# Kernel optimization log

Hardware: AMD Instinct MI355X
Metric: run time of the kernel (lower is better)

Reference implementation:

```python
import jax, jax.numpy as jnp
import numpy as np
import math

B, N, F_IN, F_OUT = 16, 2048, 256, 64


def setup_inputs() -> dict:
    key = jax.random.key(0)
    k1, k2, k3, k4 = jax.random.split(key, 4)
    x = jax.random.normal(k1, (B, N, F_IN), dtype=jnp.float32)
    adj = jax.random.randint(k2, (B, N, N), 0, 2, dtype=jnp.int32)
    stdv = 1.0 / math.sqrt(F_OUT)
    weight = jax.random.uniform(k3, (F_IN, F_OUT), dtype=jnp.float32, minval=-stdv, maxval=stdv)
    # weight2 stdv = 1/sqrt(1) = 1.0
    weight2 = jax.random.uniform(k4, (2 * F_OUT, 1), dtype=jnp.float32, minval=-1.0, maxval=1.0)
    return {"x": x, "adj": adj, "weight": weight, "weight2": weight2}


def reference(x, adj, weight, weight2):
    # h[b,n,o] = (x @ weight)  -- shared linear projection
    h = jnp.einsum("bni,io->bno", x, weight)
    Fo = weight.shape[1]
    # Split additive-attention vector: e_ij = relu(h_i . a_src + h_j . a_dst)
    # Mathematically identical to cat([h_i, h_j]) @ weight2 of the original.
    a_src = weight2[:Fo, 0]
    a_dst = weight2[Fo:, 0]
    s_src = jnp.einsum("bno,o->bn", h, a_src)  # [B, N]
    s_dst = jnp.einsum("bno,o->bn", h, a_dst)  # [B, N]
    e = jax.nn.relu(s_src[:, :, None] + s_dst[:, None, :])  # [B, N, N]
    NEG = jnp.float32(-9e15)
    scores = jnp.where(adj > 0, e, NEG)
    attention = jax.nn.softmax(scores, axis=2)  # softmax over neighbors j
    # dropout = 0.0 / eval mode -> identity
    out = jnp.einsum("bij,bjo->bio", attention, h)  # [B, N, F_OUT]
    return out
```

## Files before the change

kernel.cpp:

```cpp
#include <hip/hip_runtime.h>
#include <hip/hip_bf16.h>

#define BB 16
#define NN 2048
#define FIN 256
#define FO 64
#define PADW 264
#define CH 256

typedef __bf16 bf16x8 __attribute__((ext_vector_type(8)));
typedef __bf16 bf16x4 __attribute__((ext_vector_type(4)));
typedef float  f32x4  __attribute__((ext_vector_type(4)));
typedef int    i32x4  __attribute__((ext_vector_type(4)));

__global__ __launch_bounds__(256) void k1_gemm(
    const float* __restrict__ x, const float* __restrict__ weight,
    const float* __restrict__ w2,
    __bf16* __restrict__ hT, float* __restrict__ s_src, float* __restrict__ s_dst) {
    __shared__ __bf16 WtL[FO * PADW];
    __shared__ float vsL[FIN], vdL[FIN];
    int t = threadIdx.x;
    {
        const float4* wr = (const float4*)(weight + t * FO);
        float a = 0.f, d = 0.f;
#pragma unroll
        for (int c = 0; c < 16; ++c) {
            float4 v = wr[c];
            int o = c * 4;
            WtL[(o + 0) * PADW + t] = (__bf16)v.x;
            WtL[(o + 1) * PADW + t] = (__bf16)v.y;
            WtL[(o + 2) * PADW + t] = (__bf16)v.z;
            WtL[(o + 3) * PADW + t] = (__bf16)v.w;
            a += v.x * w2[o] + v.y * w2[o + 1] + v.z * w2[o + 2] + v.w * w2[o + 3];
            d += v.x * w2[FO + o] + v.y * w2[FO + o + 1] +
                 v.z * w2[FO + o + 2] + v.w * w2[FO + o + 3];
        }
        vsL[t] = a;
        vdL[t] = d;
    }
    __syncthreads();

    int lane = threadIdx.x & 63, w = threadIdx.x >> 6;
    int quad = lane >> 4, m = lane & 15;
    int Rbase = blockIdx.x * 64 + w * 16;
    int R = Rbase + m;
    const float* xr = x + (long)R * FIN;

    f32x4 acc[4] = {};
    float ps = 0.f, pd = 0.f;

#pragma unroll
    for (int k0 = 0; k0 < FIN; k0 += 32) {
        int kb = k0 + quad * 8;
        float4 x0 = *(const float4*)(xr + kb);
        float4 x1 = *(const float4*)(xr + kb + 4);
        float4 u0 = *(const float4*)(vsL + kb);
        float4 u1 = *(const float4*)(vsL + kb + 4);
        float4 t0 = *(const float4*)(vdL + kb);
        float4 t1 = *(const float4*)(vdL + kb + 4);
        ps += x0.x * u0.x + x0.y * u0.y + x0.z * u0.z + x0.w * u0.w +
              x1.x * u1.x + x1.y * u1.y + x1.z * u1.z + x1.w * u1.w;
        pd += x0.x * t0.x + x0.y * t0.y + x0.z * t0.z + x0.w * t0.w +
              x1.x * t1.x + x1.y * t1.y + x1.z * t1.z + x1.w * t1.w;
        bf16x8 bf = {(__bf16)x0.x, (__bf16)x0.y, (__bf16)x0.z, (__bf16)x0.w,
                     (__bf16)x1.x, (__bf16)x1.y, (__bf16)x1.z, (__bf16)x1.w};
#pragma unroll
        for (int ot = 0; ot < 4; ++ot) {
            bf16x8 af = *(const bf16x8*)(WtL + (ot * 16 + m) * PADW + kb);
            acc[ot] = __builtin_amdgcn_mfma_f32_16x16x32_bf16(af, bf, acc[ot], 0, 0, 0);
        }
    }
    ps += __shfl_xor(ps, 16);
    ps += __shfl_xor(ps, 32);
    pd += __shfl_xor(pd, 16);
    pd += __shfl_xor(pd, 32);
    if (quad == 0) {
        s_src[R] = ps;
        s_dst[R] = pd;
    }
    int b = R >> 11;
    int nb = Rbase & (NN - 1);
#pragma unroll
    for (int ot = 0; ot < 4; ++ot) {
#pragma unroll
        for (int r = 0; r < 4; ++r) {
            int o = ot * 16 + quad * 4 + r;
            hT[((long)b * FO + o) * NN + nb + m] = (__bf16)acc[ot][r];
        }
    }
}

__global__ __launch_bounds__(256) void k2_attn(
    const int* __restrict__ adj, const float* __restrict__ s_src,
    const float* __restrict__ s_dst, const __bf16* __restrict__ hT,
    float* __restrict__ out) {
    __shared__ __bf16 pbuf[4][16 * CH];
    int b = blockIdx.x >> 5;
    int i0 = (blockIdx.x & 31) << 6;
    int lane = threadIdx.x & 63, w = threadIdx.x >> 6;
    int quad = lane >> 4, m = lane & 15;
    int rowbase = i0 + w * 16;

    const float* sd = s_dst + b * NN;
    float mx = -3.0e38f;
    for (int j = lane; j < NN; j += 64) mx = fmaxf(mx, sd[j]);
#pragma unroll
    for (int off = 32; off >= 1; off >>= 1) mx = fmaxf(mx, __shfl_xor(mx, off));

    const float* ssp = s_src + b * NN + rowbase;
    const int* adjb = adj + ((long)b * NN + rowbase) * NN;
    const __bf16* hTb = hT + (long)b * FO * NN;
    __bf16* pb = pbuf[w];

    f32x4 acc[4] = {};
    f32x4 accL = {};
    const bf16x8 ones = {(__bf16)1.f, (__bf16)1.f, (__bf16)1.f, (__bf16)1.f,
                         (__bf16)1.f, (__bf16)1.f, (__bf16)1.f, (__bf16)1.f};
    int g0 = lane >> 3, u = (lane & 7) * 4;

    for (int jc = 0; jc < NN; jc += CH) {
        float4 sv = *(const float4*)(sd + jc + 4 * lane);
#pragma unroll
        for (int r = 0; r < 16; ++r) {
            float sr = ssp[r];
            float M = fmaxf(sr + mx, 0.f);
            i32x4 a0 = __builtin_nontemporal_load(
                (const i32x4*)(adjb + (long)r * NN + jc) + lane);
            float p0 = (a0.x > 0) ? __expf(fmaxf(sr + sv.x, 0.f) - M) : 0.f;
            float p1 = (a0.y > 0) ? __expf(fmaxf(sr + sv.y, 0.f) - M) : 0.f;
            float p2 = (a0.z > 0) ? __expf(fmaxf(sr + sv.z, 0.f) - M) : 0.f;
            float p3 = (a0.w > 0) ? __expf(fmaxf(sr + sv.w, 0.f) - M) : 0.f;
            bf16x4 kv = {(__bf16)p0, (__bf16)p1, (__bf16)p2, (__bf16)p3};
            *(bf16x4*)(pb + g0 * 512 + r * 32 + u) = kv;
        }
#pragma unroll
        for (int ks = 0; ks < CH / 32; ++ks) {
            bf16x8 af = *(const bf16x8*)(pb + ks * 512 + m * 32 + quad * 8);
            accL = __builtin_amdgcn_mfma_f32_16x16x32_bf16(af, ones, accL, 0, 0, 0);
            const __bf16* hb = hTb + jc + ks * 32 + quad * 8;
#pragma unroll
            for (int ot = 0; ot < 4; ++ot) {
                bf16x8 bf = *(const bf16x8*)(hb + (ot * 16 + m) * NN);
                acc[ot] = __builtin_amdgcn_mfma_f32_16x16x32_bf16(af, bf, acc[ot], 0, 0, 0);
            }
        }
    }

    float* outp = out + ((long)b * NN + rowbase) * FO;
#pragma unroll
    for (int r = 0; r < 4; ++r) {
        int orow = quad * 4 + r;
        float inv = 1.0f / accL[r];
#pragma unroll
        for (int ot = 0; ot < 4; ++ot) {
            outp[(long)orow * FO + ot * 16 + m] = acc[ot][r] * inv;
        }
    }
}

extern "C" void kernel_launch(void* const* d_in, const int* in_sizes, int n_in,
                              void* d_out, int out_size, void* d_ws, size_t ws_size,
                              hipStream_t stream) {
    const float* x      = (const float*)d_in[0];
    const int*   adj    = (const int*)d_in[1];
    const float* weight = (const float*)d_in[2];
    const float* w2     = (const float*)d_in[3];
    float* out = (float*)d_out;

    char* ws = (char*)d_ws;
    __bf16* hT   = (__bf16*)ws;
    float* s_src = (float*)(ws + 4194304);
    float* s_dst = (float*)(ws + 4194304 + 131072);

    k1_gemm<<<512, 256, 0, stream>>>(x, weight, w2, hT, s_src, s_dst);
    k2_attn<<<512, 256, 0, stream>>>(adj, s_src, s_dst, hT, out);
}
```

Before: 476.9 us.

## Pre-pack adjacency into a bitmask and compute attention probabilities directly in registers

A new streaming kernel converts the int32 adjacency matrix into a 1-bit-per-edge mask. The attention kernel then loads each row's mask once and distributes words via lane shuffles. It builds bf16 probability fragments in registers instead of staging them through LDS, and caches s_dst in shared memory. This decouples the bandwidth-heavy adjacency read from the exp/MFMA loop, at the cost of an extra kernel launch and a small mask write/read.

```diff
diff --git a/kernel.cpp b/kernel.cpp
--- a/kernel.cpp
+++ b/kernel.cpp
@@ -5,19 +5,17 @@
 #define NN 2048
 #define FIN 256
 #define FO 64
-#define PADW 264
-#define CH 256
 
 typedef __bf16 bf16x8 __attribute__((ext_vector_type(8)));
-typedef __bf16 bf16x4 __attribute__((ext_vector_type(4)));
 typedef float  f32x4  __attribute__((ext_vector_type(4)));
 typedef int    i32x4  __attribute__((ext_vector_type(4)));
+typedef unsigned int uint;
 
 __global__ __launch_bounds__(256) void k1_gemm(
     const float* __restrict__ x, const float* __restrict__ weight,
     const float* __restrict__ w2,
     __bf16* __restrict__ hT, float* __restrict__ s_src, float* __restrict__ s_dst) {
-    __shared__ __bf16 WtL[FO * PADW];
+    __shared__ __bf16 WtL[FO * 264];
     __shared__ float vsL[FIN], vdL[FIN];
     int t = threadIdx.x;
     {
@@ -27,10 +25,10 @@
         for (int c = 0; c < 16; ++c) {
             float4 v = wr[c];
             int o = c * 4;
-            WtL[(o + 0) * PADW + t] = (__bf16)v.x;
-            WtL[(o + 1) * PADW + t] = (__bf16)v.y;
-            WtL[(o + 2) * PADW + t] = (__bf16)v.z;
-            WtL[(o + 3) * PADW + t] = (__bf16)v.w;
+            WtL[(o + 0) * 264 + t] = (__bf16)v.x;
+            WtL[(o + 1) * 264 + t] = (__bf16)v.y;
+            WtL[(o + 2) * 264 + t] = (__bf16)v.z;
+            WtL[(o + 3) * 264 + t] = (__bf16)v.w;
             a += v.x * w2[o] + v.y * w2[o + 1] + v.z * w2[o + 2] + v.w * w2[o + 3];
             d += v.x * w2[FO + o] + v.y * w2[FO + o + 1] +
                  v.z * w2[FO + o + 2] + v.w * w2[FO + o + 3];
@@ -66,7 +64,7 @@
                      (__bf16)x1.x, (__bf16)x1.y, (__bf16)x1.z, (__bf16)x1.w};
 #pragma unroll
         for (int ot = 0; ot < 4; ++ot) {
-            bf16x8 af = *(const bf16x8*)(WtL + (ot * 16 + m) * PADW + kb);
+            bf16x8 af = *(const bf16x8*)(WtL + (ot * 16 + m) * 264 + kb);
             acc[ot] = __builtin_amdgcn_mfma_f32_16x16x32_bf16(af, bf, acc[ot], 0, 0, 0);
         }
     }
@@ -90,54 +88,80 @@
     }
 }
 
+__global__ __launch_bounds__(256) void k_pack(const int* __restrict__ adj,
+                                              unsigned char* __restrict__ mask) {
+    size_t t = (size_t)blockIdx.x * 256 + threadIdx.x;
+    const i32x4* ap = (const i32x4*)(adj + t * 8);
+    i32x4 a0 = __builtin_nontemporal_load(ap);
+    i32x4 a1 = __builtin_nontemporal_load(ap + 1);
+    unsigned b = (unsigned)(a0.x > 0) | ((unsigned)(a0.y > 0) << 1) |
+                 ((unsigned)(a0.z > 0) << 2) | ((unsigned)(a0.w > 0) << 3) |
+                 ((unsigned)(a1.x > 0) << 4) | ((unsigned)(a1.y > 0) << 5) |
+                 ((unsigned)(a1.z > 0) << 6) | ((unsigned)(a1.w > 0) << 7);
+    mask[t] = (unsigned char)b;
+}
+
 __global__ __launch_bounds__(256) void k2_attn(
-    const int* __restrict__ adj, const float* __restrict__ s_src,
+    const unsigned char* __restrict__ mask, const float* __restrict__ s_src,
     const float* __restrict__ s_dst, const __bf16* __restrict__ hT,
     float* __restrict__ out) {
-    __shared__ __bf16 pbuf[4][16 * CH];
+    __shared__ float sdL[NN];
     int b = blockIdx.x >> 5;
     int i0 = (blockIdx.x & 31) << 6;
-    int lane = threadIdx.x & 63, w = threadIdx.x >> 6;
+    int lane = threadIdx.x & 63;
+    int w = threadIdx.x >> 6;
     int quad = lane >> 4, m = lane & 15;
     int rowbase = i0 + w * 16;
 
-    const float* sd = s_dst + b * NN;
+    {
+        const float4* sp = (const float4*)(s_dst + b * NN);
+        float4* dp = (float4*)sdL;
+        for (int t = threadIdx.x; t < NN / 4; t += 256) dp[t] = sp[t];
+    }
+    __syncthreads();
+
     float mx = -3.0e38f;
-    for (int j = lane; j < NN; j += 64) mx = fmaxf(mx, sd[j]);
+    for (int j = lane; j < NN; j += 64) mx = fmaxf(mx, sdL[j]);
 #pragma unroll
     for (int off = 32; off >= 1; off >>= 1) mx = fmaxf(mx, __shfl_xor(mx, off));
 
-    const float* ssp = s_src + b * NN + rowbase;
-    const int* adjb = adj + ((long)b * NN + rowbase) * NN;
+    float ssr = s_src[b * NN + rowbase + m];
+    float M = fmaxf(ssr + mx, 0.f);
+
+    const uint4* mp = (const uint4*)(mask + ((size_t)(b * NN + rowbase + m)) * 256 +
+                                     quad * 64);
+    uint4 mw0 = mp[0], mw1 = mp[1], mw2 = mp[2], mw3 = mp[3];
+    uint dw[16] = {mw0.x, mw0.y, mw0.z, mw0.w, mw1.x, mw1.y, mw1.z, mw1.w,
+                   mw2.x, mw2.y, mw2.z, mw2.w, mw3.x, mw3.y, mw3.z, mw3.w};
+
     const __bf16* hTb = hT + (long)b * FO * NN;
-    __bf16* pb = pbuf[w];
-
     f32x4 acc[4] = {};
     f32x4 accL = {};
     const bf16x8 ones = {(__bf16)1.f, (__bf16)1.f, (__bf16)1.f, (__bf16)1.f,
                          (__bf16)1.f, (__bf16)1.f, (__bf16)1.f, (__bf16)1.f};
-    int g0 = lane >> 3, u = (lane & 7) * 4;
-
-    for (int jc = 0; jc < NN; jc += CH) {
-        float4 sv = *(const float4*)(sd + jc + 4 * lane);
-#pragma unroll
-        for (int r = 0; r < 16; ++r) {
-            float sr = ssp[r];
-            float M = fmaxf(sr + mx, 0.f);
-            i32x4 a0 = __builtin_nontemporal_load(
-                (const i32x4*)(adjb + (long)r * NN + jc) + lane);
-            float p0 = (a0.x > 0) ? __expf(fmaxf(sr + sv.x, 0.f) - M) : 0.f;
-            float p1 = (a0.y > 0) ? __expf(fmaxf(sr + sv.y, 0.f) - M) : 0.f;
-            float p2 = (a0.z > 0) ? __expf(fmaxf(sr + sv.z, 0.f) - M) : 0.f;
-            float p3 = (a0.w > 0) ? __expf(fmaxf(sr + sv.w, 0.f) - M) : 0.f;
-            bf16x4 kv = {(__bf16)p0, (__bf16)p1, (__bf16)p2, (__bf16)p3};
-            *(bf16x4*)(pb + g0 * 512 + r * 32 + u) = kv;
-        }
-#pragma unroll
-        for (int ks = 0; ks < CH / 32; ++ks) {
-            bf16x8 af = *(const bf16x8*)(pb + ks * 512 + m * 32 + quad * 8);
+    int q8 = quad * 8;
+
+    for (int qo = 0; qo < 4; ++qo) {
+        int src = (qo << 4) | m;
+#pragma unroll
+        for (int u = 0; u < 16; ++u) {
+            int ks = (qo << 4) | u;
+            uint mv = (uint)__shfl((int)dw[u], src);
+            const float* sp = sdL + ks * 32 + q8;
+            float4 s0 = *(const float4*)sp;
+            float4 s1 = *(const float4*)(sp + 4);
+            float p0 = ((mv >> (q8 + 0)) & 1) ? __expf(fmaxf(ssr + s0.x, 0.f) - M) : 0.f;
+            float p1 = ((mv >> (q8 + 1)) & 1) ? __expf(fmaxf(ssr + s0.y, 0.f) - M) : 0.f;
+            float p2 = ((mv >> (q8 + 2)) & 1) ? __expf(fmaxf(ssr + s0.z, 0.f) - M) : 0.f;
+            float p3 = ((mv >> (q8 + 3)) & 1) ? __expf(fmaxf(ssr + s0.w, 0.f) - M) : 0.f;
+            float p4 = ((mv >> (q8 + 4)) & 1) ? __expf(fmaxf(ssr + s1.x, 0.f) - M) : 0.f;
+            float p5 = ((mv >> (q8 + 5)) & 1) ? __expf(fmaxf(ssr + s1.y, 0.f) - M) : 0.f;
+            float p6 = ((mv >> (q8 + 6)) & 1) ? __expf(fmaxf(ssr + s1.z, 0.f) - M) : 0.f;
+            float p7 = ((mv >> (q8 + 7)) & 1) ? __expf(fmaxf(ssr + s1.w, 0.f) - M) : 0.f;
+            bf16x8 af = {(__bf16)p0, (__bf16)p1, (__bf16)p2, (__bf16)p3,
+                         (__bf16)p4, (__bf16)p5, (__bf16)p6, (__bf16)p7};
             accL = __builtin_amdgcn_mfma_f32_16x16x32_bf16(af, ones, accL, 0, 0, 0);
-            const __bf16* hb = hTb + jc + ks * 32 + quad * 8;
+            const __bf16* hb = hTb + ks * 32 + q8;
 #pragma unroll
             for (int ot = 0; ot < 4; ++ot) {
                 bf16x8 bf = *(const bf16x8*)(hb + (ot * 16 + m) * NN);
@@ -171,7 +195,9 @@
     __bf16* hT   = (__bf16*)ws;
     float* s_src = (float*)(ws + 4194304);
     float* s_dst = (float*)(ws + 4194304 + 131072);
-
+    unsigned char* mask = (unsigned char*)(ws + 4194304 + 262144);
+
+    k_pack<<<32768, 256, 0, stream>>>(adj, mask);
     k1_gemm<<<512, 256, 0, stream>>>(x, weight, w2, hT, s_src, s_dst);
-    k2_attn<<<512, 256, 0, stream>>>(adj, s_src, s_dst, hT, out);
-}
+    k2_attn<<<512, 256, 0, stream>>>(mask, s_src, s_dst, hT, out);
+}
```

New measurement: 428.5 us. 10.2% less time.

## Factor softmax exponent into precomputed per-column exps and build MFMA A-fragments in registers

Applied to the files above, without the earlier changes.

Rewrites the attention kernel so each lane computes its own row's probabilities directly in MFMA A-operand layout. The LDS staging buffer is removed, and adjacency is packed into bitmasks loaded in groups of four. The per-element exp is replaced by max(K*exp(s_dst-mx), exp(-M)), using a shared table of exp(s_dst-mx) computed once per block in LDS, which removes most transcendental work. It also adds an occupancy hint of 2 blocks per SM; the factored form may differ slightly numerically and uses more registers.

```diff
diff --git a/kernel.cpp b/kernel.cpp
--- a/kernel.cpp
+++ b/kernel.cpp
@@ -5,19 +5,17 @@
 #define NN 2048
 #define FIN 256
 #define FO 64
-#define PADW 264
-#define CH 256
 
 typedef __bf16 bf16x8 __attribute__((ext_vector_type(8)));
-typedef __bf16 bf16x4 __attribute__((ext_vector_type(4)));
 typedef float  f32x4  __attribute__((ext_vector_type(4)));
 typedef int    i32x4  __attribute__((ext_vector_type(4)));
+typedef unsigned int uint;
 
 __global__ __launch_bounds__(256) void k1_gemm(
     const float* __restrict__ x, const float* __restrict__ weight,
     const float* __restrict__ w2,
     __bf16* __restrict__ hT, float* __restrict__ s_src, float* __restrict__ s_dst) {
-    __shared__ __bf16 WtL[FO * PADW];
+    __shared__ __bf16 WtL[FO * 264];
     __shared__ float vsL[FIN], vdL[FIN];
     int t = threadIdx.x;
     {
@@ -27,10 +25,10 @@
         for (int c = 0; c < 16; ++c) {
             float4 v = wr[c];
             int o = c * 4;
-            WtL[(o + 0) * PADW + t] = (__bf16)v.x;
-            WtL[(o + 1) * PADW + t] = (__bf16)v.y;
-            WtL[(o + 2) * PADW + t] = (__bf16)v.z;
-            WtL[(o + 3) * PADW + t] = (__bf16)v.w;
+            WtL[(o + 0) * 264 + t] = (__bf16)v.x;
+            WtL[(o + 1) * 264 + t] = (__bf16)v.y;
+            WtL[(o + 2) * 264 + t] = (__bf16)v.z;
+            WtL[(o + 3) * 264 + t] = (__bf16)v.w;
             a += v.x * w2[o] + v.y * w2[o + 1] + v.z * w2[o + 2] + v.w * w2[o + 3];
             d += v.x * w2[FO + o] + v.y * w2[FO + o + 1] +
                  v.z * w2[FO + o + 2] + v.w * w2[FO + o + 3];
@@ -66,7 +64,7 @@
                      (__bf16)x1.x, (__bf16)x1.y, (__bf16)x1.z, (__bf16)x1.w};
 #pragma unroll
         for (int ot = 0; ot < 4; ++ot) {
-            bf16x8 af = *(const bf16x8*)(WtL + (ot * 16 + m) * PADW + kb);
+            bf16x8 af = *(const bf16x8*)(WtL + (ot * 16 + m) * 264 + kb);
             acc[ot] = __builtin_amdgcn_mfma_f32_16x16x32_bf16(af, bf, acc[ot], 0, 0, 0);
         }
     }
@@ -90,54 +88,80 @@
     }
 }
 
-__global__ __launch_bounds__(256) void k2_attn(
+__global__ __launch_bounds__(256, 2) void k2_attn(
     const int* __restrict__ adj, const float* __restrict__ s_src,
     const float* __restrict__ s_dst, const __bf16* __restrict__ hT,
     float* __restrict__ out) {
-    __shared__ __bf16 pbuf[4][16 * CH];
+    __shared__ float EL[NN];
     int b = blockIdx.x >> 5;
     int i0 = (blockIdx.x & 31) << 6;
     int lane = threadIdx.x & 63, w = threadIdx.x >> 6;
     int quad = lane >> 4, m = lane & 15;
     int rowbase = i0 + w * 16;
+    int row = rowbase + m;
 
     const float* sd = s_dst + b * NN;
     float mx = -3.0e38f;
     for (int j = lane; j < NN; j += 64) mx = fmaxf(mx, sd[j]);
 #pragma unroll
     for (int off = 32; off >= 1; off >>= 1) mx = fmaxf(mx, __shfl_xor(mx, off));
-
-    const float* ssp = s_src + b * NN + rowbase;
-    const int* adjb = adj + ((long)b * NN + rowbase) * NN;
+    for (int t = lane; t < NN; t += 64) EL[t] = __expf(sd[t] - mx);
+
+    float ssr = s_src[b * NN + row];
+    float T = ssr + mx;
+    float M = fmaxf(T, 0.f);
+    float K = __expf(fminf(T, 0.f));
+    float cM = __expf(-M);
+
+    const int* adjrow = adj + ((long)(b * NN + row)) * NN;
     const __bf16* hTb = hT + (long)b * FO * NN;
-    __bf16* pb = pbuf[w];
+    int q8 = quad * 8;
 
     f32x4 acc[4] = {};
     f32x4 accL = {};
     const bf16x8 ones = {(__bf16)1.f, (__bf16)1.f, (__bf16)1.f, (__bf16)1.f,
                          (__bf16)1.f, (__bf16)1.f, (__bf16)1.f, (__bf16)1.f};
-    int g0 = lane >> 3, u = (lane & 7) * 4;
-
-    for (int jc = 0; jc < NN; jc += CH) {
-        float4 sv = *(const float4*)(sd + jc + 4 * lane);
-#pragma unroll
-        for (int r = 0; r < 16; ++r) {
-            float sr = ssp[r];
-            float M = fmaxf(sr + mx, 0.f);
-            i32x4 a0 = __builtin_nontemporal_load(
-                (const i32x4*)(adjb + (long)r * NN + jc) + lane);
-            float p0 = (a0.x > 0) ? __expf(fmaxf(sr + sv.x, 0.f) - M) : 0.f;
-            float p1 = (a0.y > 0) ? __expf(fmaxf(sr + sv.y, 0.f) - M) : 0.f;
-            float p2 = (a0.z > 0) ? __expf(fmaxf(sr + sv.z, 0.f) - M) : 0.f;
-            float p3 = (a0.w > 0) ? __expf(fmaxf(sr + sv.w, 0.f) - M) : 0.f;
-            bf16x4 kv = {(__bf16)p0, (__bf16)p1, (__bf16)p2, (__bf16)p3};
-            *(bf16x4*)(pb + g0 * 512 + r * 32 + u) = kv;
-        }
-#pragma unroll
-        for (int ks = 0; ks < CH / 32; ++ks) {
-            bf16x8 af = *(const bf16x8*)(pb + ks * 512 + m * 32 + quad * 8);
+    uint bw[16];
+
+#pragma unroll
+    for (int g = 0; g < 4; ++g) {
+#pragma unroll
+        for (int ii = 0; ii < 4; ++ii) {
+            int i = g * 4 + ii;
+            uint bwv = 0;
+#pragma unroll
+            for (int j = 0; j < 4; ++j) {
+                int ks = i * 4 + j;
+                const i32x4* ap = (const i32x4*)(adjrow + ks * 32 + q8);
+                i32x4 a0 = __builtin_nontemporal_load(ap);
+                i32x4 a1 = __builtin_nontemporal_load(ap + 1);
+                uint by = (uint)(a0.x > 0) | ((uint)(a0.y > 0) << 1) |
+                          ((uint)(a0.z > 0) << 2) | ((uint)(a0.w > 0) << 3) |
+                          ((uint)(a1.x > 0) << 4) | ((uint)(a1.y > 0) << 5) |
+                          ((uint)(a1.z > 0) << 6) | ((uint)(a1.w > 0) << 7);
+                bwv |= by << (8 * j);
+            }
+            bw[i] = bwv;
+        }
+#pragma unroll
+        for (int u = 0; u < 16; ++u) {
+            int ks = g * 16 + u;
+            uint mb = (bw[g * 4 + (u >> 2)] >> ((u & 3) * 8)) & 0xffu;
+            const float* ep = EL + ks * 32 + q8;
+            float4 e0 = *(const float4*)ep;
+            float4 e1 = *(const float4*)(ep + 4);
+            float p0 = (mb & 1u)   ? fmaxf(K * e0.x, cM) : 0.f;
+            float p1 = (mb & 2u)   ? fmaxf(K * e0.y, cM) : 0.f;
+            float p2 = (mb & 4u)   ? fmaxf(K * e0.z, cM) : 0.f;
+            float p3 = (mb & 8u)   ? fmaxf(K * e0.w, cM) : 0.f;
+            float p4 = (mb & 16u)  ? fmaxf(K * e1.x, cM) : 0.f;
+            float p5 = (mb & 32u)  ? fmaxf(K * e1.y, cM) : 0.f;
+            float p6 = (mb & 64u)  ? fmaxf(K * e1.z, cM) : 0.f;
+            float p7 = (mb & 128u) ? fmaxf(K * e1.w, cM) : 0.f;
+            bf16x8 af = {(__bf16)p0, (__bf16)p1, (__bf16)p2, (__bf16)p3,
+                         (__bf16)p4, (__bf16)p5, (__bf16)p6, (__bf16)p7};
             accL = __builtin_amdgcn_mfma_f32_16x16x32_bf16(af, ones, accL, 0, 0, 0);
-            const __bf16* hb = hTb + jc + ks * 32 + quad * 8;
+            const __bf16* hb = hTb + ks * 32 + q8;
 #pragma unroll
             for (int ot = 0; ot < 4; ++ot) {
                 bf16x8 bf = *(const bf16x8*)(hb + (ot * 16 + m) * NN);
```

Result: faster. 437.6 us (-8.2%).
